# Performance work log

Measured on AMD Instinct MI355X. Metric: run time of the kernel, lower is better.

## Reference

```python
import jax, jax.numpy as jnp
import numpy as np

N = 2048
D_T = 256; D_F = 256
E_T = 32; E_F = 32; E_C = 128
C = 5; Q = 512


def setup_inputs() -> dict:
    key = jax.random.key(0)
    ks = jax.random.split(key, 12)
    # full graph minus self-loops, row-major (matches dense_to_sparse ordering)
    r, c = np.meshgrid(np.arange(N), np.arange(N), indexing='ij')
    m = r != c
    edge_index = jnp.asarray(np.stack([r[m], c[m]]), dtype=jnp.int32)  # [2, N*(N-1)]
    E = edge_index.shape[1]
    s = 0.02
    return {
        'time_features': jax.random.normal(ks[0], (N, D_T), jnp.float32),
        'edge_index': edge_index,
        'time_edge_weight': jax.random.uniform(ks[1], (E,), jnp.float32),
        'freq_features': jax.random.normal(ks[2], (N, D_F), jnp.float32),
        'freq_edge_weight': jax.random.uniform(ks[3], (E,), jnp.float32),
        'labels': jax.random.randint(ks[4], (N,), 0, C, jnp.int32),
        'num_classes': C,
        'query_size': Q,
        'Wt': jax.random.normal(ks[5], (D_T, E_T), jnp.float32) * s,
        'bt': jnp.zeros((E_T,), jnp.float32),
        'Wf': jax.random.normal(ks[6], (D_F, E_F), jnp.float32) * s,
        'bf': jnp.zeros((E_F,), jnp.float32),
        'Wc': jax.random.normal(ks[7], (E_T + E_F + C, E_C), jnp.float32) * s,
        'bc': jnp.zeros((E_C,), jnp.float32),
        'Wo': jax.random.normal(ks[8], (E_C, C), jnp.float32) * s,
        'bo': jnp.zeros((C,), jnp.float32),
    }


def _gcn(x, A, W, b):
    # torch_geometric GCNConv: D^{-1/2}(A + I)D^{-1/2} (X W) + b
    n = A.shape[0]
    Ah = A + jnp.eye(n, dtype=A.dtype)
    deg = Ah.sum(axis=1)
    dis = jnp.where(deg > 0, jax.lax.rsqrt(deg), 0.0)
    return (dis[:, None] * Ah * dis[None, :]) @ (x @ W) + b


def reference(time_features, edge_index, time_edge_weight, freq_features,
              freq_edge_weight, labels, num_classes, query_size,
              Wt, bt, Wf, bf, Wc, bc, Wo, bo):
    n = time_features.shape[0]
    lrelu = lambda z: jax.nn.leaky_relu(z, 0.01)

    def dense_adj(w):  # A[dst, src] = w
        return jnp.zeros((n, n), w.dtype).at[edge_index[1], edge_index[0]].add(w)

    te = lrelu(_gcn(time_features, dense_adj(time_edge_weight), Wt, bt))
    fe = lrelu(_gcn(freq_features, dense_adj(freq_edge_weight), Wf, bf))

    # to_one_hot: one_hot[:n - query_size, labels] = 1 -> support rows get 1 in
    # every column that appears anywhere in `labels`
    cols = jnp.zeros((num_classes,), te.dtype).at[labels].set(1.0)
    rowmask = (jnp.arange(n) < (n - query_size)).astype(te.dtype)
    one_hot = rowmask[:, None] * cols[None, :]

    feats = jnp.concatenate([te, fe, one_hot], axis=-1)  # [n, E_T+E_F+C]

    # graph_construction (no_grad in original): 1 / (L1 distance over the
    # non-one-hot dims + 1e-5), zero diagonal
    fd = jax.lax.stop_gradient(feats[:, : feats.shape[1] - num_classes])
    dist = jnp.sum(jnp.abs(fd[:, None, :] - fd[None, :, :]), axis=-1)  # [n, n]
    Aw = (1.0 / (dist + 1e-5)) * (1.0 - jnp.eye(n, dtype=feats.dtype))

    emb = lrelu(_gcn(feats, Aw, Wc, bc))
    return emb @ Wo + bo
```

## Files before the change

kernel.cpp:

```cpp
#include <hip/hip_runtime.h>
#include <hip/hip_bf16.h>

#define N 2048
#define NM1 2047
#define DT 256
#define ET 32
#define EC 128
#define NC 5
#define FS 80
#define FD 69
#define KC_ET 16
#define KC_EC 16

typedef unsigned short u16;
typedef unsigned int u32;
typedef float f32x4 __attribute__((ext_vector_type(4)));
typedef __bf16 bf16x8 __attribute__((ext_vector_type(8)));

__device__ inline u16 bf16_rne(float x){
    unsigned int b = __float_as_uint(x);
    b += 0x7fffu + ((b >> 16) & 1u);
    return (u16)(b >> 16);
}
__device__ inline float bf16_to_f(u16 h){
    return __uint_as_float(((unsigned int)h) << 16);
}
__device__ inline f32x4 mfma16x16x32(bf16x8 a, bf16x8 b, f32x4 c){
    return __builtin_amdgcn_mfma_f32_16x16x32_bf16(a, b, c, 0, 0, 0);
}

__global__ __launch_bounds__(256) void k_deg_label_xw(const float* __restrict__ tw,
                                                      const float* __restrict__ fw,
                                                      const int* __restrict__ labels,
                                                      const float* __restrict__ Xt,
                                                      const float* __restrict__ Wt,
                                                      const float* __restrict__ Xf,
                                                      const float* __restrict__ Wf,
                                                      float* __restrict__ degT,
                                                      float* __restrict__ degF,
                                                      float* __restrict__ cols,
                                                      float* __restrict__ Yt,
                                                      float* __restrict__ Yf){
    int b = blockIdx.x;
    int t = threadIdx.x;
    if (b < 512){
        int p = (b & 7)*256 + t;
        if (p >= NM1) return;
        int s0 = (b >> 3)*32;
        float lowT=0.f, highT=0.f, lowF=0.f, highF=0.f;
        #pragma unroll 8
        for (int r = 0; r < 32; ++r){
            int s = s0 + r;
            float vt = tw[(size_t)s*NM1 + p];
            float vf = fw[(size_t)s*NM1 + p];
            if (s <= p){ highT += vt; highF += vf; }
            else       { lowT  += vt; lowF  += vf; }
        }
        atomicAdd(&degT[p],   lowT);
        atomicAdd(&degF[p],   lowF);
        atomicAdd(&degT[p+1], highT);
        atomicAdd(&degF[p+1], highF);
        return;
    }
    if (b == 512){
        __shared__ float lc[NC];
        if (t < NC) lc[t] = 0.f;
        __syncthreads();
        for (int i = t; i < N; i += 256){
            int l = labels[i];
            if (l >= 0 && l < NC) lc[l] = 1.f;
        }
        __syncthreads();
        if (t < NC) cols[t] = lc[t];
        return;
    }
    int idx = b - 513;
    const float* X = (idx & 256) ? Xf : Xt;
    const float* W = (idx & 256) ? Wf : Wt;
    float*       Y = (idx & 256) ? Yf : Yt;
    __shared__ float Ws[DT*ET];
    __shared__ float Xs[8*DT];
    for (int j = t; j < DT*ET; j += 256) Ws[j] = W[j];
    int i0 = (idx & 255)*8;
    for (int j = t; j < 8*DT; j += 256) Xs[j] = X[(size_t)i0*DT + j];
    __syncthreads();
    int r = t >> 5, f = t & 31;
    const float* xr = Xs + r*DT;
    float acc = 0.f;
    #pragma unroll 8
    for (int d = 0; d < DT; ++d) acc += xr[d]*Ws[d*ET+f];
    Y[(size_t)(i0+r)*ET+f] = acc;
}

__global__ __launch_bounds__(256) void k_agg_et_m2(const float* __restrict__ tw,
                                                   const float* __restrict__ fw,
                                                   const float* __restrict__ Yt,
                                                   const float* __restrict__ Yf,
                                                   const float* __restrict__ degT,
                                                   const float* __restrict__ degF,
                                                   float* __restrict__ Pt,
                                                   float* __restrict__ Pf){
    __shared__ u16 Zs[2][32][136];
    __shared__ u16 As[2][64][72];
    int t = threadIdx.x;
    int w = t >> 6, l = t & 63, lr = l & 15, lg = l >> 4;
    int i0 = blockIdx.x*64;
    int kc = blockIdx.y;
    int k0 = kc*128;

    for (int g = 0; g < 2; ++g){
        const float* A   = g ? fw   : tw;
        const float* Y   = g ? Yf   : Yt;
        const float* deg = g ? degF : degT;
        float*       P   = g ? Pf   : Pt;

        __syncthreads();
        {
            int f = t >> 3;
            int kb16 = (t & 7)*16;
            u16 h8[16], l8[16];
            #pragma unroll
            for (int j = 0; j < 16; ++j){
                int k = k0 + kb16 + j;
                float rd = rsqrtf(1.f + deg[k]);
                float v = rd * Y[(size_t)k*ET + f];
                u16 h = bf16_rne(v);
                h8[j] = h;
                l8[j] = bf16_rne(v - bf16_to_f(h));
            }
            uint4 pk;
            pk.x = (u32)h8[0] | ((u32)h8[1]<<16);
            pk.y = (u32)h8[2] | ((u32)h8[3]<<16);
            pk.z = (u32)h8[4] | ((u32)h8[5]<<16);
            pk.w = (u32)h8[6] | ((u32)h8[7]<<16);
            *(uint4*)&Zs[0][f][kb16] = pk;
            pk.x = (u32)h8[8]  | ((u32)h8[9]<<16);
            pk.y = (u32)h8[10] | ((u32)h8[11]<<16);
            pk.z = (u32)h8[12] | ((u32)h8[13]<<16);
            pk.w = (u32)h8[14] | ((u32)h8[15]<<16);
            *(uint4*)&Zs[0][f][kb16+8] = pk;
            pk.x = (u32)l8[0] | ((u32)l8[1]<<16);
            pk.y = (u32)l8[2] | ((u32)l8[3]<<16);
            pk.z = (u32)l8[4] | ((u32)l8[5]<<16);
            pk.w = (u32)l8[6] | ((u32)l8[7]<<16);
            *(uint4*)&Zs[1][f][kb16] = pk;
            pk.x = (u32)l8[8]  | ((u32)l8[9]<<16);
            pk.y = (u32)l8[10] | ((u32)l8[11]<<16);
            pk.z = (u32)l8[12] | ((u32)l8[13]<<16);
            pk.w = (u32)l8[14] | ((u32)l8[15]<<16);
            *(uint4*)&Zs[1][f][kb16+8] = pk;
        }

        f32x4 acc[2];
        acc[0] = (f32x4){0.f,0.f,0.f,0.f};
        acc[1] = (f32x4){0.f,0.f,0.f,0.f};

        for (int sub = 0; sub < 2; ++sub){
            int kbs = k0 + sub*64;
            __syncthreads();
            #pragma unroll
            for (int e = 0; e < 8; ++e){
                int id = t + e*256;
                int kp  = id >> 6;
                int i_l = id & 63;
                int k  = kbs + kp*2;
                int gi = i0 + i_l;
                float v0 = 0.f, v1 = 0.f;
                if (gi != k)   v0 = A[(size_t)k*NM1 + gi - (gi > k ? 1 : 0)];
                if (gi != k+1) v1 = A[(size_t)(k+1)*NM1 + gi - (gi > k+1 ? 1 : 0)];
                u16 h0 = bf16_rne(v0);
                u16 l0 = bf16_rne(v0 - bf16_to_f(h0));
                u16 h1 = bf16_rne(v1);
                u16 l1 = bf16_rne(v1 - bf16_to_f(h1));
                *(u32*)&As[0][i_l][kp*2] = (u32)h0 | ((u32)h1<<16);
                *(u32*)&As[1][i_l][kp*2] = (u32)l0 | ((u32)l1<<16);
            }
            __syncthreads();
            #pragma unroll
            for (int ks = 0; ks < 2; ++ks){
                bf16x8 aH = *(const bf16x8*)&As[0][w*16 + lr][ks*32 + lg*8];
                bf16x8 aL = *(const bf16x8*)&As[1][w*16 + lr][ks*32 + lg*8];
                #pragma unroll
                for (int cf = 0; cf < 2; ++cf){
                    bf16x8 bH = *(const bf16x8*)&Zs[0][cf*16 + lr][sub*64 + ks*32 + lg*8];
                    bf16x8 bL = *(const bf16x8*)&Zs[1][cf*16 + lr][sub*64 + ks*32 + lg*8];
                    acc[cf] = mfma16x16x32(aH, bH, acc[cf]);
                    acc[cf] = mfma16x16x32(aL, bH, acc[cf]);
                    acc[cf] = mfma16x16x32(aH, bL, acc[cf]);
                }
            }
        }
        #pragma unroll
        for (int cf = 0; cf < 2; ++cf)
            #pragma unroll
            for (int r = 0; r < 4; ++r){
                int gi = i0 + w*16 + lg*4 + r;
                P[(size_t)kc*(N*ET) + (size_t)gi*ET + cf*16 + lr] = acc[cf][r];
            }
    }
}

__global__ __launch_bounds__(256) void k_feats_epi(const float* __restrict__ Pt,
                                                   const float* __restrict__ Pf,
                                                   const float* __restrict__ Yt,
                                                   const float* __restrict__ Yf,
                                                   const float* __restrict__ degT,
                                                   const float* __restrict__ degF,
                                                   const float* __restrict__ bt,
                                                   const float* __restrict__ bfv,
                                                   const float* __restrict__ cols,
                                                   const int* __restrict__ qsize,
                                                   float* __restrict__ feats){
    int idx = blockIdx.x*256 + threadIdx.x;
    int i = idx >> 6;
    int f = idx & 63;
    float s, rd, b;
    if (f < ET){
        rd = rsqrtf(1.f + degT[i]);
        s = rd*Yt[(size_t)i*ET + f];
        #pragma unroll
        for (int kc = 0; kc < KC_ET; ++kc) s += Pt[(size_t)kc*(N*ET) + (size_t)i*ET + f];
        b = bt[f];
    } else {
        int g = f - ET;
        rd = rsqrtf(1.f + degF[i]);
        s = rd*Yf[(size_t)i*ET + g];
        #pragma unroll
        for (int kc = 0; kc < KC_ET; ++kc) s += Pf[(size_t)kc*(N*ET) + (size_t)i*ET + g];
        b = bfv[g];
    }
    float v = rd*s + b;
    feats[(size_t)i*FS + f] = v > 0.f ? v : 0.01f*v;
    if (f < NC){
        int nsup = N - qsize[0];
        feats[(size_t)i*FS + 2*ET + f] = (i < nsup) ? cols[f] : 0.f;
    }
}

__global__ __launch_bounds__(256) void k_aw_zc(const float* __restrict__ feats,
                                               const float* __restrict__ Wc,
                                               u16* __restrict__ Aw_hi,
                                               u16* __restrict__ Aw_lo,
                                               u16* __restrict__ ZcT_hi,
                                               u16* __restrict__ ZcT_lo,
                                               float* __restrict__ dsum){
    __shared__ __align__(16) char sm[37632];
    int t = threadIdx.x;
    int b = blockIdx.x;
    if (b < 1024){
        float* fiT = (float*)sm;
        float* fjT = fiT + 64*68;
        int i0 = (b & 31)*64, j0 = (b >> 5)*64;
        {
            int row = t >> 2;
            int cb  = (t & 3)*16;
            const float4* si = (const float4*)(feats + (size_t)(i0+row)*FS + cb);
            const float4* sj = (const float4*)(feats + (size_t)(j0+row)*FS + cb);
            #pragma unroll
            for (int s = 0; s < 4; ++s){
                float4 v = si[s];
                float4 w = sj[s];
                int c = cb + s*4;
                fiT[(c+0)*68+row]=v.x; fiT[(c+1)*68+row]=v.y; fiT[(c+2)*68+row]=v.z; fiT[(c+3)*68+row]=v.w;
                fjT[(c+0)*68+row]=w.x; fjT[(c+1)*68+row]=w.y; fjT[(c+2)*68+row]=w.z; fjT[(c+3)*68+row]=w.w;
            }
        }
        __syncthreads();
        int tx = t & 15, ty = t >> 4;
        float acc[4][4];
        #pragma unroll
        for (int u=0;u<4;++u)
            #pragma unroll
            for (int v=0;v<4;++v) acc[u][v]=0.f;
        for (int d = 0; d < 64; ++d){
            float4 a4 = *(const float4*)&fiT[d*68 + ty*4];
            float4 b4 = *(const float4*)&fjT[d*68 + tx*4];
            const float* ap = (const float*)&a4;
            const float* bp = (const float*)&b4;
            #pragma unroll
            for (int u = 0; u < 4; ++u)
                #pragma unroll
                for (int v = 0; v < 4; ++v)
                    acc[u][v] += fabsf(ap[u]-bp[v]);
        }
        #pragma unroll
        for (int u = 0; u < 4; ++u){
            int gi = i0 + ty*4 + u;
            float po[4];
            u16 hh[4], ll[4];
            #pragma unroll
            for (int v = 0; v < 4; ++v){
                int gj = j0 + tx*4 + v;
                float w = (gi==gj) ? 1.0f : 1.0f/(acc[u][v] + 1e-5f);
                po[v] = w;
                u16 h = bf16_rne(w);
                hh[v] = h;
                ll[v] = bf16_rne(w - bf16_to_f(h));
            }
            uint2 ph, pl;
            ph.x = (u32)hh[0] | ((u32)hh[1]<<16);
            ph.y = (u32)hh[2] | ((u32)hh[3]<<16);
            pl.x = (u32)ll[0] | ((u32)ll[1]<<16);
            pl.y = (u32)ll[2] | ((u32)ll[3]<<16);
            *(uint2*)&Aw_hi[(size_t)gi*N + j0 + tx*4] = ph;
            *(uint2*)&Aw_lo[(size_t)gi*N + j0 + tx*4] = pl;
            float rs = (po[0]+po[1]) + (po[2]+po[3]);
            rs += __shfl_xor(rs, 1);
            rs += __shfl_xor(rs, 2);
            rs += __shfl_xor(rs, 4);
            rs += __shfl_xor(rs, 8);
            if (tx == 0) atomicAdd(&dsum[gi], rs);
        }
        return;
    }
    {
        float* Wcs = (float*)sm;
        float* fr  = Wcs + FD*EC;
        int idx = b - 1024;
        int i0 = idx*8;
        for (int j = t; j < FD*EC; j += 256) Wcs[j] = Wc[j];
        for (int j = t; j < 8*FD; j += 256){
            int r = j / FD;
            int c = j - r*FD;
            fr[r*72 + c] = feats[(size_t)(i0+r)*FS + c];
        }
        __syncthreads();
        int f  = t & 127;
        int rh = t >> 7;
        u16 hh[4], ll[4];
        #pragma unroll
        for (int rr = 0; rr < 4; ++rr){
            int r = rh*4 + rr;
            float acc = 0.f;
            #pragma unroll
            for (int d = 0; d < FD; ++d) acc += fr[r*72+d]*Wcs[d*EC+f];
            u16 h = bf16_rne(acc);
            hh[rr] = h;
            ll[rr] = bf16_rne(acc - bf16_to_f(h));
        }
        uint2 ph, pl;
        ph.x = (u32)hh[0] | ((u32)hh[1]<<16);
        ph.y = (u32)hh[2] | ((u32)hh[3]<<16);
        pl.x = (u32)ll[0] | ((u32)ll[1]<<16);
        pl.y = (u32)ll[2] | ((u32)ll[3]<<16);
        *(uint2*)&ZcT_hi[(size_t)f*N + i0 + rh*4] = ph;
        *(uint2*)&ZcT_lo[(size_t)f*N + i0 + rh*4] = pl;
    }
}

__global__ __launch_bounds__(256) void k_agg_ec(const u16* __restrict__ Aw_hi,
                                                const u16* __restrict__ Aw_lo,
                                                const u16* __restrict__ ZcT_hi,
                                                const u16* __restrict__ ZcT_lo,
                                                const float* __restrict__ dsum,
                                                float* __restrict__ Pe){
    __shared__ u16 Ah[64*72];
    __shared__ u16 Al[64*72];
    __shared__ u16 Zh[128*72];
    __shared__ u16 Zl[128*72];
    int t = threadIdx.x;
    int w  = t >> 6;
    int l  = t & 63;
    int lr = l & 15;
    int lg = l >> 4;
    int i0 = blockIdx.x*64;
    int kb0 = blockIdx.y*128;
    f32x4 acc[8];
    #pragma unroll
    for (int tt = 0; tt < 8; ++tt) acc[tt] = (f32x4){0.f, 0.f, 0.f, 0.f};

    for (int sub = 0; sub < 2; ++sub){
        int kbs = kb0 + sub*64;
        #pragma unroll
        for (int e = 0; e < 2; ++e){
            int id = t + e*256;
            int row = id >> 3, ch = (id & 7)*8;
            uint4 vh = *(const uint4*)&Aw_hi[(size_t)(i0+row)*N + kbs + ch];
            uint4 vl = *(const uint4*)&Aw_lo[(size_t)(i0+row)*N + kbs + ch];
            const u16* ph = (const u16*)&vh;
            const u16* pl = (const u16*)&vl;
            u16 nh[8], nl[8];
            #pragma unroll
            for (int j = 0; j < 8; ++j){
                float a = bf16_to_f(ph[j]) + bf16_to_f(pl[j]);
                float v = a * rsqrtf(dsum[kbs + ch + j]);
                u16 h = bf16_rne(v);
                nh[j] = h;
                nl[j] = bf16_rne(v - bf16_to_f(h));
            }
            uint4 oh, ol;
            oh.x = (u32)nh[0] | ((u32)nh[1]<<16);
            oh.y = (u32)nh[2] | ((u32)nh[3]<<16);
            oh.z = (u32)nh[4] | ((u32)nh[5]<<16);
            oh.w = (u32)nh[6] | ((u32)nh[7]<<16);
            ol.x = (u32)nl[0] | ((u32)nl[1]<<16);
            ol.y = (u32)nl[2] | ((u32)nl[3]<<16);
            ol.z = (u32)nl[4] | ((u32)nl[5]<<16);
            ol.w = (u32)nl[6] | ((u32)nl[7]<<16);
            *(uint4*)&Ah[row*72 + ch] = oh;
            *(uint4*)&Al[row*72 + ch] = ol;
        }
        #pragma unroll
        for (int e = 0; e < 4; ++e){
            int id = t + e*256;
            int row = id >> 3, ch = (id & 7)*8;
            uint4 vh = *(const uint4*)&ZcT_hi[(size_t)row*N + kbs + ch];
            uint4 vl = *(const uint4*)&ZcT_lo[(size_t)row*N + kbs + ch];
            *(uint4*)&Zh[row*72 + ch] = vh;
            *(uint4*)&Zl[row*72 + ch] = vl;
        }
        __syncthreads();
        #pragma unroll
        for (int ks = 0; ks < 2; ++ks){
            int aoff = (w*16 + lr)*72 + ks*32 + lg*8;
            bf16x8 aH = *(const bf16x8*)&Ah[aoff];
            bf16x8 aL = *(const bf16x8*)&Al[aoff];
            #pragma unroll
            for (int tt = 0; tt < 8; ++tt){
                int zoff = (tt*16 + lr)*72 + ks*32 + lg*8;
                bf16x8 bH = *(const bf16x8*)&Zh[zoff];
                bf16x8 bL = *(const bf16x8*)&Zl[zoff];
                acc[tt] = mfma16x16x32(aH, bH, acc[tt]);
                acc[tt] = mfma16x16x32(aL, bH, acc[tt]);
                acc[tt] = mfma16x16x32(aH, bL, acc[tt]);
            }
        }
        __syncthreads();
    }
    #pragma unroll
    for (int tt = 0; tt < 8; ++tt){
        #pragma unroll
        for (int r = 0; r < 4; ++r){
            int gi = i0 + w*16 + lg*4 + r;
            Pe[(size_t)blockIdx.y*(N*EC) + (size_t)gi*EC + tt*16 + lr] = acc[tt][r];
        }
    }
}

__global__ __launch_bounds__(256) void k_embfinal(const float* __restrict__ Pe,
                                                  const float* __restrict__ dsum,
                                                  const float* __restrict__ bc,
                                                  const float* __restrict__ Wo,
                                                  const float* __restrict__ bo,
                                                  float* __restrict__ out){
    __shared__ float vs[2][EC];
    __shared__ float Wos[EC*NC];
    __shared__ float bos[NC];
    int t = threadIdx.x;
    for (int idx = t; idx < EC*NC; idx += 256) Wos[idx] = Wo[idx];
    if (t < NC) bos[t] = bo[t];
    int rr = t >> 7, f = t & 127;
    int i = blockIdx.x*2 + rr;
    size_t idx = (size_t)i*EC + f;
    float s = 0.f;
    #pragma unroll
    for (int kc = 0; kc < KC_EC; ++kc) s += Pe[(size_t)kc*(N*EC) + idx];
    float v = rsqrtf(dsum[i])*s + bc[f];
    vs[rr][f] = v > 0.f ? v : 0.01f*v;
    __syncthreads();
    if (t < 2*NC){
        int r = t / NC;
        int c = t - r*NC;
        float a = bos[c];
        #pragma unroll 8
        for (int f2 = 0; f2 < EC; ++f2) a += vs[r][f2]*Wos[f2*NC+c];
        out[(size_t)(blockIdx.x*2 + r)*NC + c] = a;
    }
}

extern "C" void kernel_launch(void* const* d_in, const int* in_sizes, int n_in,
                              void* d_out, int out_size, void* d_ws, size_t ws_size,
                              hipStream_t stream) {
    const float* time_features = (const float*)d_in[0];
    const float* tw            = (const float*)d_in[2];
    const float* freq_features = (const float*)d_in[3];
    const float* fw            = (const float*)d_in[4];
    const int*   labels        = (const int*)d_in[5];
    const int*   qsize         = (const int*)d_in[7];
    const float* Wt  = (const float*)d_in[8];
    const float* bt  = (const float*)d_in[9];
    const float* Wf  = (const float*)d_in[10];
    const float* bfv = (const float*)d_in[11];
    const float* Wc  = (const float*)d_in[12];
    const float* bc  = (const float*)d_in[13];
    const float* Wo  = (const float*)d_in[14];
    const float* bo  = (const float*)d_in[15];
    float* out = (float*)d_out;

    float* ws    = (float*)d_ws;
    float* degT  = ws;
    float* degF  = degT + N;
    float* dsum  = degF + N;
    float* colsb = dsum + N;
    float* Yt    = colsb + 8;
    float* Yf    = Yt + (size_t)N*ET;
    float* feats = Yf + (size_t)N*ET;
    float* Zc    = feats + (size_t)N*FS;
    float* Aw    = Zc + (size_t)N*EC;
    float* Pt    = Aw + (size_t)N*N;
    float* Pf    = Pt + (size_t)KC_ET*N*ET;
    float* Pe    = Pf + (size_t)KC_ET*N*ET;

    u16* ZcT_hi = (u16*)Zc;
    u16* ZcT_lo = ZcT_hi + (size_t)N*EC;
    u16* Aw_hi  = (u16*)Aw;
    u16* Aw_lo  = Aw_hi + (size_t)N*N;

    hipMemsetAsync(degT, 0, 3*N*sizeof(float), stream);
    k_deg_label_xw<<<1025, 256, 0, stream>>>(tw, fw, labels,
                                             time_features, Wt, freq_features, Wf,
                                             degT, degF, colsb, Yt, Yf);
    k_agg_et_m2<<<dim3(N/64, KC_ET), 256, 0, stream>>>(tw, fw, Yt, Yf, degT, degF, Pt, Pf);
    k_feats_epi<<<(N*64)/256, 256, 0, stream>>>(Pt, Pf, Yt, Yf, degT, degF,
                                                bt, bfv, colsb, qsize, feats);
    k_aw_zc<<<1280, 256, 0, stream>>>(feats, Wc, Aw_hi, Aw_lo, ZcT_hi, ZcT_lo, dsum);
    k_agg_ec<<<dim3(N/64, KC_EC), 256, 0, stream>>>(Aw_hi, Aw_lo, ZcT_hi, ZcT_lo, dsum, Pe);
    k_embfinal<<<N/2, 256, 0, stream>>>(Pe, dsum, bc, Wo, bo, out);
}
```

Measured before the change: 197.2 us.

## Split edge-aggregation graphs across waves and halve feature tile in EC aggregation

The first-layer aggregation kernel now processes both graphs at once: waves 0-1 handle the time graph and waves 2-3 the frequency graph, each over 32 rows. Each wave loads its adjacency values straight from global memory into registers and splits them into bf16 hi/lo there, which removes the shared-memory A staging and its barriers. This doubles the grid size and raises parallelism, but the per-lane global loads are strided by row and less coalesced. The EC aggregation kernel is also split into two 64-feature halves to double block count and cut shared memory and accumulator registers, at the cost of loading the Aw tile twice.

```diff
diff --git a/kernel.cpp b/kernel.cpp
--- a/kernel.cpp
+++ b/kernel.cpp
@@ -92,32 +92,29 @@
     Y[(size_t)(i0+r)*ET+f] = acc;
 }
 
-__global__ __launch_bounds__(256) void k_agg_et_m2(const float* __restrict__ tw,
-                                                   const float* __restrict__ fw,
-                                                   const float* __restrict__ Yt,
-                                                   const float* __restrict__ Yf,
-                                                   const float* __restrict__ degT,
-                                                   const float* __restrict__ degF,
-                                                   float* __restrict__ Pt,
-                                                   float* __restrict__ Pf){
-    __shared__ u16 Zs[2][32][136];
-    __shared__ u16 As[2][64][72];
+__global__ __launch_bounds__(256) void k_agg_et_m(const float* __restrict__ tw,
+                                                  const float* __restrict__ fw,
+                                                  const float* __restrict__ Yt,
+                                                  const float* __restrict__ Yf,
+                                                  const float* __restrict__ degT,
+                                                  const float* __restrict__ degF,
+                                                  float* __restrict__ Pt,
+                                                  float* __restrict__ Pf){
+    __shared__ u16 Zs[2][2][32][136];
     int t = threadIdx.x;
     int w = t >> 6, l = t & 63, lr = l & 15, lg = l >> 4;
-    int i0 = blockIdx.x*64;
+    int g = w >> 1, wh = w & 1;
+    int i0 = blockIdx.x*32;
     int kc = blockIdx.y;
     int k0 = kc*128;
 
-    for (int g = 0; g < 2; ++g){
-        const float* A   = g ? fw   : tw;
-        const float* Y   = g ? Yf   : Yt;
-        const float* deg = g ? degF : degT;
-        float*       P   = g ? Pf   : Pt;
-
-        __syncthreads();
-        {
-            int f = t >> 3;
-            int kb16 = (t & 7)*16;
+    {
+        int f = t >> 3;
+        int kb16 = (t & 7)*16;
+        #pragma unroll
+        for (int gg = 0; gg < 2; ++gg){
+            const float* Y   = gg ? Yf   : Yt;
+            const float* deg = gg ? degF : degT;
             u16 h8[16], l8[16];
             #pragma unroll
             for (int j = 0; j < 16; ++j){
@@ -133,71 +130,77 @@
             pk.y = (u32)h8[2] | ((u32)h8[3]<<16);
             pk.z = (u32)h8[4] | ((u32)h8[5]<<16);
             pk.w = (u32)h8[6] | ((u32)h8[7]<<16);
-            *(uint4*)&Zs[0][f][kb16] = pk;
+            *(uint4*)&Zs[gg][0][f][kb16] = pk;
             pk.x = (u32)h8[8]  | ((u32)h8[9]<<16);
             pk.y = (u32)h8[10] | ((u32)h8[11]<<16);
             pk.z = (u32)h8[12] | ((u32)h8[13]<<16);
             pk.w = (u32)h8[14] | ((u32)h8[15]<<16);
-            *(uint4*)&Zs[0][f][kb16+8] = pk;
+            *(uint4*)&Zs[gg][0][f][kb16+8] = pk;
             pk.x = (u32)l8[0] | ((u32)l8[1]<<16);
             pk.y = (u32)l8[2] | ((u32)l8[3]<<16);
             pk.z = (u32)l8[4] | ((u32)l8[5]<<16);
             pk.w = (u32)l8[6] | ((u32)l8[7]<<16);
-            *(uint4*)&Zs[1][f][kb16] = pk;
+            *(uint4*)&Zs[gg][1][f][kb16] = pk;
             pk.x = (u32)l8[8]  | ((u32)l8[9]<<16);
             pk.y = (u32)l8[10] | ((u32)l8[11]<<16);
             pk.z = (u32)l8[12] | ((u32)l8[13]<<16);
             pk.w = (u32)l8[14] | ((u32)l8[15]<<16);
-            *(uint4*)&Zs[1][f][kb16+8] = pk;
-        }
-
-        f32x4 acc[2];
-        acc[0] = (f32x4){0.f,0.f,0.f,0.f};
-        acc[1] = (f32x4){0.f,0.f,0.f,0.f};
-
-        for (int sub = 0; sub < 2; ++sub){
-            int kbs = k0 + sub*64;
-            __syncthreads();
-            #pragma unroll
-            for (int e = 0; e < 8; ++e){
-                int id = t + e*256;
-                int kp  = id >> 6;
-                int i_l = id & 63;
-                int k  = kbs + kp*2;
-                int gi = i0 + i_l;
-                float v0 = 0.f, v1 = 0.f;
-                if (gi != k)   v0 = A[(size_t)k*NM1 + gi - (gi > k ? 1 : 0)];
-                if (gi != k+1) v1 = A[(size_t)(k+1)*NM1 + gi - (gi > k+1 ? 1 : 0)];
-                u16 h0 = bf16_rne(v0);
-                u16 l0 = bf16_rne(v0 - bf16_to_f(h0));
-                u16 h1 = bf16_rne(v1);
-                u16 l1 = bf16_rne(v1 - bf16_to_f(h1));
-                *(u32*)&As[0][i_l][kp*2] = (u32)h0 | ((u32)h1<<16);
-                *(u32*)&As[1][i_l][kp*2] = (u32)l0 | ((u32)l1<<16);
-            }
-            __syncthreads();
-            #pragma unroll
-            for (int ks = 0; ks < 2; ++ks){
-                bf16x8 aH = *(const bf16x8*)&As[0][w*16 + lr][ks*32 + lg*8];
-                bf16x8 aL = *(const bf16x8*)&As[1][w*16 + lr][ks*32 + lg*8];
-                #pragma unroll
-                for (int cf = 0; cf < 2; ++cf){
-                    bf16x8 bH = *(const bf16x8*)&Zs[0][cf*16 + lr][sub*64 + ks*32 + lg*8];
-                    bf16x8 bL = *(const bf16x8*)&Zs[1][cf*16 + lr][sub*64 + ks*32 + lg*8];
-                    acc[cf] = mfma16x16x32(aH, bH, acc[cf]);
-                    acc[cf] = mfma16x16x32(aL, bH, acc[cf]);
-                    acc[cf] = mfma16x16x32(aH, bL, acc[cf]);
-                }
-            }
-        }
-        #pragma unroll
-        for (int cf = 0; cf < 2; ++cf)
-            #pragma unroll
-            for (int r = 0; r < 4; ++r){
-                int gi = i0 + w*16 + lg*4 + r;
-                P[(size_t)kc*(N*ET) + (size_t)gi*ET + cf*16 + lr] = acc[cf][r];
-            }
-    }
+            *(uint4*)&Zs[gg][1][f][kb16+8] = pk;
+        }
+    }
+    __syncthreads();
+
+    const float* A = g ? fw : tw;
+    f32x4 acc[2];
+    acc[0] = (f32x4){0.f,0.f,0.f,0.f};
+    acc[1] = (f32x4){0.f,0.f,0.f,0.f};
+
+    for (int sub = 0; sub < 2; ++sub){
+        int kb = k0 + sub*64;
+        int row = i0 + wh*16 + lr;
+        #pragma unroll
+        for (int ks = 0; ks < 2; ++ks){
+            int kbase = kb + ks*32 + lg*8;
+            u16 ah[8], al[8];
+            #pragma unroll
+            for (int j = 0; j < 8; ++j){
+                int k = kbase + j;
+                float v = 0.f;
+                if (row != k) v = A[(size_t)k*NM1 + row - (row > k ? 1 : 0)];
+                u16 h = bf16_rne(v);
+                ah[j] = h;
+                al[j] = bf16_rne(v - bf16_to_f(h));
+            }
+            uint4 pa, pb;
+            pa.x = (u32)ah[0] | ((u32)ah[1]<<16);
+            pa.y = (u32)ah[2] | ((u32)ah[3]<<16);
+            pa.z = (u32)ah[4] | ((u32)ah[5]<<16);
+            pa.w = (u32)ah[6] | ((u32)ah[7]<<16);
+            pb.x = (u32)al[0] | ((u32)al[1]<<16);
+            pb.y = (u32)al[2] | ((u32)al[3]<<16);
+            pb.z = (u32)al[4] | ((u32)al[5]<<16);
+            pb.w = (u32)al[6] | ((u32)al[7]<<16);
+            bf16x8 aH = *(bf16x8*)&pa;
+            bf16x8 aL = *(bf16x8*)&pb;
+            int koff = sub*64 + ks*32 + lg*8;
+            #pragma unroll
+            for (int ff = 0; ff < 2; ++ff){
+                bf16x8 bH = *(const bf16x8*)&Zs[g][0][ff*16+lr][koff];
+                bf16x8 bL = *(const bf16x8*)&Zs[g][1][ff*16+lr][koff];
+                acc[ff] = mfma16x16x32(aH, bH, acc[ff]);
+                acc[ff] = mfma16x16x32(aL, bH, acc[ff]);
+                acc[ff] = mfma16x16x32(aH, bL, acc[ff]);
+            }
+        }
+    }
+    float* P = g ? Pf : Pt;
+    #pragma unroll
+    for (int ff = 0; ff < 2; ++ff)
+        #pragma unroll
+        for (int r = 0; r < 4; ++r){
+            int gi = i0 + wh*16 + lg*4 + r;
+            P[(size_t)kc*(N*ET) + (size_t)gi*ET + ff*16 + lr] = acc[ff][r];
+        }
 }
 
 __global__ __launch_bounds__(256) void k_feats_epi(const float* __restrict__ Pt,
@@ -356,18 +359,19 @@
                                                 float* __restrict__ Pe){
     __shared__ u16 Ah[64*72];
     __shared__ u16 Al[64*72];
-    __shared__ u16 Zh[128*72];
-    __shared__ u16 Zl[128*72];
+    __shared__ u16 Zh[64*72];
+    __shared__ u16 Zl[64*72];
     int t = threadIdx.x;
     int w  = t >> 6;
     int l  = t & 63;
     int lr = l & 15;
     int lg = l >> 4;
-    int i0 = blockIdx.x*64;
+    int i0 = (blockIdx.x >> 1)*64;
+    int fh = blockIdx.x & 1;
     int kb0 = blockIdx.y*128;
-    f32x4 acc[8];
+    f32x4 acc[4];
     #pragma unroll
-    for (int tt = 0; tt < 8; ++tt) acc[tt] = (f32x4){0.f, 0.f, 0.f, 0.f};
+    for (int tt = 0; tt < 4; ++tt) acc[tt] = (f32x4){0.f, 0.f, 0.f, 0.f};
 
     for (int sub = 0; sub < 2; ++sub){
         int kbs = kb0 + sub*64;
@@ -401,11 +405,11 @@
             *(uint4*)&Al[row*72 + ch] = ol;
         }
         #pragma unroll
-        for (int e = 0; e < 4; ++e){
+        for (int e = 0; e < 2; ++e){
             int id = t + e*256;
             int row = id >> 3, ch = (id & 7)*8;
-            uint4 vh = *(const uint4*)&ZcT_hi[(size_t)row*N + kbs + ch];
-            uint4 vl = *(const uint4*)&ZcT_lo[(size_t)row*N + kbs + ch];
+            uint4 vh = *(const uint4*)&ZcT_hi[(size_t)(fh*64 + row)*N + kbs + ch];
+            uint4 vl = *(const uint4*)&ZcT_lo[(size_t)(fh*64 + row)*N + kbs + ch];
             *(uint4*)&Zh[row*72 + ch] = vh;
             *(uint4*)&Zl[row*72 + ch] = vl;
         }
@@ -416,7 +420,7 @@
             bf16x8 aH = *(const bf16x8*)&Ah[aoff];
             bf16x8 aL = *(const bf16x8*)&Al[aoff];
             #pragma unroll
-            for (int tt = 0; tt < 8; ++tt){
+            for (int tt = 0; tt < 4; ++tt){
                 int zoff = (tt*16 + lr)*72 + ks*32 + lg*8;
                 bf16x8 bH = *(const bf16x8*)&Zh[zoff];
                 bf16x8 bL = *(const bf16x8*)&Zl[zoff];
@@ -428,11 +432,11 @@
         __syncthreads();
     }
     #pragma unroll
-    for (int tt = 0; tt < 8; ++tt){
+    for (int tt = 0; tt < 4; ++tt){
         #pragma unroll
         for (int r = 0; r < 4; ++r){
             int gi = i0 + w*16 + lg*4 + r;
-            Pe[(size_t)blockIdx.y*(N*EC) + (size_t)gi*EC + tt*16 + lr] = acc[tt][r];
+            Pe[(size_t)blockIdx.y*(N*EC) + (size_t)gi*EC + fh*64 + tt*16 + lr] = acc[tt][r];
         }
     }
 }
@@ -510,10 +514,10 @@
     k_deg_label_xw<<<1025, 256, 0, stream>>>(tw, fw, labels,
                                              time_features, Wt, freq_features, Wf,
                                              degT, degF, colsb, Yt, Yf);
-    k_agg_et_m2<<<dim3(N/64, KC_ET), 256, 0, stream>>>(tw, fw, Yt, Yf, degT, degF, Pt, Pf);
+    k_agg_et_m<<<dim3(N/32, KC_ET), 256, 0, stream>>>(tw, fw, Yt, Yf, degT, degF, Pt, Pf);
     k_feats_epi<<<(N*64)/256, 256, 0, stream>>>(Pt, Pf, Yt, Yf, degT, degF,
                                                 bt, bfv, colsb, qsize, feats);
     k_aw_zc<<<1280, 256, 0, stream>>>(feats, Wc, Aw_hi, Aw_lo, ZcT_hi, ZcT_lo, dsum);
-    k_agg_ec<<<dim3(N/64, KC_EC), 256, 0, stream>>>(Aw_hi, Aw_lo, ZcT_hi, ZcT_lo, dsum, Pe);
+    k_agg_ec<<<dim3(64, KC_EC), 256, 0, stream>>>(Aw_hi, Aw_lo, ZcT_hi, ZcT_lo, dsum, Pe);
     k_embfinal<<<N/2, 256, 0, stream>>>(Pe, dsum, bc, Wo, bo, out);
 }
```

Result: no change. 196.7 us (-0.2%).
